# Kernel optimization log

Measured on AMD Instinct MI355X. Metric: run time of the kernel, lower is better.

## Reference

```python
import jax, jax.numpy as jnp
import numpy as np

ALPHA = 0.1
BETA = float(np.log(0.5 / 4 + 1.0))  # theta=0.5, layer=4


def setup_inputs() -> dict:
    key = jax.random.key(0)
    k = jax.random.split(key, 6)
    B, C, N, K = 1, 128, 40000, 16
    x = jax.random.normal(k[0], (B, C, N, 1), dtype=jnp.float32)
    x_0 = jax.random.normal(k[1], (B, N, C), dtype=jnp.float32)
    edge_index = jax.random.randint(k[2], (2, B, N, K), 0, N)
    W1 = jax.random.normal(k[3], (C, C), dtype=jnp.float32) * 0.05
    W2 = jax.random.normal(k[4], (C, C), dtype=jnp.float32) * 0.05
    bias = jax.random.uniform(k[5], (1, 1, C), dtype=jnp.float32)
    return {"x": x, "x_0": x_0, "edge_index": edge_index, "W1": W1, "W2": W2, "bias": bias}


def reference(x, x_0, edge_index, W1, W2, bias):
    # x: [B, C, N, 1]; x_0: [B, N, C]; edge_index: [2, B, N, K]
    B, C, N, _ = x.shape
    idx = edge_index[0]  # neighbor indices [B, N, K]
    self_idx = jnp.broadcast_to(jnp.arange(N, dtype=idx.dtype)[None, :, None], (B, N, 1))
    idx = jnp.concatenate([idx, self_idx], axis=-1)  # add self loops -> [B, N, K+1]
    deg = idx.shape[-1]  # constant degree K+1
    x2 = x[..., 0]  # [B, C, N]
    # irregular gather of neighbor features: [B, C, N, K+1]
    x_j = jax.vmap(lambda xb, ib: xb[:, ib])(x2, idx)
    aggr = x_j.sum(axis=-1) * (1.0 / deg)  # [B, C, N]
    aggr = jnp.swapaxes(aggr, 1, 2)  # [B, N, C]
    out = (aggr * ((1.0 - ALPHA) * (1.0 - BETA))
           + jnp.einsum('bnc,oc->bno', aggr, W1) * BETA
           + x_0 * (ALPHA * (1.0 - BETA))
           + jnp.einsum('bnc,oc->bno', x_0, W2) * BETA
           + bias)
    out = jax.nn.relu(out)
    return jnp.swapaxes(out, 1, 2)[..., None]  # [B, C, N, 1]
```

## Files before the change

### kernel.cpp

```cpp
#include <hip/hip_runtime.h>

#define N_NODES 40000
#define C_DIM   128
#define K_NBR   16

static constexpr float BETA_F = 0.11778303565638346f;
static constexpr float C1_F   = 0.7939952679092549f;
static constexpr float C2_F   = 0.08822169643436166f;

typedef __attribute__((ext_vector_type(8))) short bf16x8;
typedef __attribute__((ext_vector_type(4))) float f32x4;

__device__ __forceinline__ unsigned pack_bf16x2(float a, float b) {
    unsigned ua = __float_as_uint(a), ub = __float_as_uint(b);
    ua += 0x7fffu + ((ua >> 16) & 1u);
    ub += 0x7fffu + ((ub >> 16) & 1u);
    return (ua >> 16) | (ub & 0xffff0000u);
}
__device__ __forceinline__ float bflo(unsigned u) { return __uint_as_float(u << 16); }
__device__ __forceinline__ float bfhi(unsigned u) { return __uint_as_float(u & 0xffff0000u); }

__global__ void build_wfrag_kernel(const float* __restrict__ W1,
                                   const float* __restrict__ W2,
                                   unsigned short* __restrict__ WB) {
    int i = blockIdx.x * 256 + threadIdx.x;
    int frag   = i >> 9;
    int within = i & 511;
    int lane = within >> 3, j = within & 7;
    int otile = frag >> 3, kblk = frag & 7;
    int o = otile * 16 + (lane & 15);
    int c = kblk * 32 + ((lane >> 4) << 3) + j;
    float w = (c < 128) ? W1[o * 128 + c] : W2[o * 128 + c - 128];
    unsigned u = __float_as_uint(w);
    u += 0x7fffu + ((u >> 16) & 1u);
    WB[i] = (unsigned short)(u >> 16);
}

__global__ __launch_bounds__(256) void transpose_cast_kernel(
        const float* __restrict__ x, unsigned* __restrict__ xTb) {
    __shared__ float tile[32][33];
    const int nb = blockIdx.x * 32;
    const int cb = blockIdx.y * 32;
    const int tid = threadIdx.x;
    const int tx = tid & 31, ty = tid >> 5;
#pragma unroll
    for (int i = 0; i < 32; i += 8)
        tile[ty + i][tx] = x[(size_t)(cb + ty + i) * N_NODES + nb + tx];
    __syncthreads();
    const int nl = tid >> 3;
    const int cp = tid & 7;
#pragma unroll
    for (int it = 0; it < 2; ++it) {
        int cpl = cp + 8 * it;
        float a = tile[2 * cpl][nl];
        float b = tile[2 * cpl + 1][nl];
        xTb[(size_t)(nb + nl) * 64 + (cb >> 1) + cpl] = pack_bf16x2(a, b);
    }
}

__global__ __launch_bounds__(256) void fused2_kernel(
        const unsigned* __restrict__ xTb,
        const float*    __restrict__ x0,
        const int*      __restrict__ e0,
        const bf16x8*   __restrict__ WB,
        const float*    __restrict__ bias,
        float*          __restrict__ out) {
    __shared__ unsigned y[32][132];
    __shared__ int eis[512];

    const int nb   = blockIdx.x * 32;
    const int tid  = threadIdx.x;
    const int lane = tid & 63;
    const int wid  = tid >> 6;

    eis[tid]       = e0[(size_t)nb * K_NBR + tid];
    eis[256 + tid] = e0[(size_t)nb * K_NBR + 256 + tid];
    __syncthreads();

    const float inv_deg = 1.0f / 17.0f;
#pragma unroll 1
    for (int s = 0; s < 8; ++s) {
        const int local = wid * 8 + s;
        const int n = nb + local;
        unsigned u = xTb[(size_t)n * 64 + lane];
        float a0 = bflo(u), a1 = bfhi(u);
        const int* ep = &eis[local * K_NBR];
#pragma unroll
        for (int k = 0; k < K_NBR; ++k) {
            const int j = ep[k];
            unsigned v = xTb[(size_t)j * 64 + lane];
            a0 += bflo(v);
            a1 += bfhi(v);
        }
        y[local][lane] = pack_bf16x2(a0 * inv_deg, a1 * inv_deg);
        const float2 xv = *(const float2*)&x0[(size_t)n * C_DIM + 2 * lane];
        y[local][64 + lane] = pack_bf16x2(xv.x, xv.y);
    }
    __syncthreads();

    const int nh = wid & 1;
    const int oh = wid >> 1;
    const int arow = nh * 16 + (lane & 15);
    const int acol = (lane >> 4) * 4;

    bf16x8 afrag[8];
#pragma unroll
    for (int kb = 0; kb < 8; ++kb)
        afrag[kb] = *(const bf16x8*)&y[arow][kb * 16 + acol];

    f32x4 acc[4];
#pragma unroll
    for (int t = 0; t < 4; ++t) {
        f32x4 a = {0.f, 0.f, 0.f, 0.f};
#pragma unroll
        for (int kb = 0; kb < 8; ++kb) {
            bf16x8 b = WB[((oh * 4 + t) * 8 + kb) * 64 + lane];
            a = __builtin_amdgcn_mfma_f32_16x16x32_bf16(afrag[kb], b, a, 0, 0, 0);
        }
        acc[t] = a;
    }

    const int rbase = nh * 16 + (lane >> 4) * 4;
#pragma unroll
    for (int t = 0; t < 4; ++t) {
        const int o = oh * 64 + t * 16 + (lane & 15);
        const float bo = bias[o];
        const int oc = o >> 1;
        const bool hi = (o & 1) != 0;
        float res[4];
#pragma unroll
        for (int r = 0; r < 4; ++r) {
            const int row = rbase + r;
            const unsigned ua = y[row][oc];
            const unsigned ux = y[row][64 + oc];
            const float aggr = hi ? bfhi(ua) : bflo(ua);
            const float x0v  = hi ? bfhi(ux) : bflo(ux);
            float v = fmaf(acc[t][r], BETA_F,
                      fmaf(aggr, C1_F,
                      fmaf(x0v,  C2_F, bo)));
            res[r] = v > 0.0f ? v : 0.0f;
        }
        *(float4*)&out[(size_t)o * N_NODES + nb + rbase] =
            make_float4(res[0], res[1], res[2], res[3]);
    }
}

extern "C" void kernel_launch(void* const* d_in, const int* in_sizes, int n_in,
                              void* d_out, int out_size, void* d_ws, size_t ws_size,
                              hipStream_t stream) {
    const float* x    = (const float*)d_in[0];
    const float* x0   = (const float*)d_in[1];
    const int*   ei   = (const int*)  d_in[2];
    const float* W1   = (const float*)d_in[3];
    const float* W2   = (const float*)d_in[4];
    const float* bias = (const float*)d_in[5];
    float* out = (float*)d_out;

    unsigned short* WB  = (unsigned short*)d_ws;
    unsigned*       xTb = (unsigned*)((char*)d_ws + 65536);

    hipLaunchKernelGGL(build_wfrag_kernel, dim3(128), dim3(256), 0, stream,
                       W1, W2, WB);
    hipLaunchKernelGGL(transpose_cast_kernel, dim3(1250, 4), dim3(256), 0, stream,
                       x, xTb);
    hipLaunchKernelGGL(fused2_kernel, dim3(1250), dim3(256), 0, stream,
                       xTb, x0, ei, (const bf16x8*)WB, bias, out);
}
```

Before: 45.92 us.

## Fold scaling constants into weights, merge prep kernels, widen gather loads

Folds BETA, the 1/17 degree normalization and the C1/C2 identity terms into the bf16 weight matrix, so the epilogue reduces to bias plus ReLU and no longer rereads aggr/x0 from shared memory. Merges the weight-fragment build and the transpose-cast into one prep kernel, removing a launch, and uses float4 loads and uint4 stores for the transpose. In the fused kernel, each half-wave now gathers a separate node with 8-byte loads. Folding the identity terms into bf16 weights lowers the precision of the residual paths, and the single weight-building block may lengthen the prep kernel's tail.

Measured after the change: 67.94 us. +48.0%, slower.

```diff
diff --git a/kernel.cpp b/kernel.cpp
--- a/kernel.cpp
+++ b/kernel.cpp
@@ -4,9 +4,10 @@
 #define C_DIM   128
 #define K_NBR   16
 
-static constexpr float BETA_F = 0.11778303565638346f;
-static constexpr float C1_F   = 0.7939952679092549f;
-static constexpr float C2_F   = 0.08822169643436166f;
+static constexpr float BETA_F  = 0.11778303565638346f;
+static constexpr float C1_F    = 0.7939952679092549f;
+static constexpr float C2_F    = 0.08822169643436166f;
+static constexpr float INV_DEG = 1.0f / 17.0f;
 
 typedef __attribute__((ext_vector_type(8))) short bf16x8;
 typedef __attribute__((ext_vector_type(4))) float f32x4;
@@ -20,45 +21,68 @@
 __device__ __forceinline__ float bflo(unsigned u) { return __uint_as_float(u << 16); }
 __device__ __forceinline__ float bfhi(unsigned u) { return __uint_as_float(u & 0xffff0000u); }
 
-__global__ void build_wfrag_kernel(const float* __restrict__ W1,
-                                   const float* __restrict__ W2,
-                                   unsigned short* __restrict__ WB) {
-    int i = blockIdx.x * 256 + threadIdx.x;
-    int frag   = i >> 9;
-    int within = i & 511;
-    int lane = within >> 3, j = within & 7;
-    int otile = frag >> 3, kblk = frag & 7;
-    int o = otile * 16 + (lane & 15);
-    int c = kblk * 32 + ((lane >> 4) << 3) + j;
-    float w = (c < 128) ? W1[o * 128 + c] : W2[o * 128 + c - 128];
-    unsigned u = __float_as_uint(w);
-    u += 0x7fffu + ((u >> 16) & 1u);
-    WB[i] = (unsigned short)(u >> 16);
+__global__ __launch_bounds__(256) void prep_kernel(
+        const float* __restrict__ x,
+        const float* __restrict__ W1,
+        const float* __restrict__ W2,
+        unsigned* __restrict__ xTb,
+        unsigned short* __restrict__ WB) {
+    __shared__ unsigned tile[64][68];
+
+    if (blockIdx.x == 625) {
+        const int tid = threadIdx.x;
+#pragma unroll 4
+        for (int it = 0; it < 128; ++it) {
+            int i = it * 256 + tid;
+            int frag = i >> 9, within = i & 511;
+            int lane = within >> 3, j = within & 7;
+            int otile = frag >> 3, kblk = frag & 7;
+            int o = otile * 16 + (lane & 15);
+            int c = kblk * 32 + ((lane >> 4) << 3) + j;
+            float v;
+            if (c < 128) {
+                v = (BETA_F * W1[o * 128 + c] + (c == o ? C1_F : 0.0f)) * INV_DEG;
+            } else {
+                int c2 = c - 128;
+                v = BETA_F * W2[o * 128 + c2] + (c2 == o ? C2_F : 0.0f);
+            }
+            unsigned u = __float_as_uint(v);
+            u += 0x7fffu + ((u >> 16) & 1u);
+            WB[i] = (unsigned short)(u >> 16);
+        }
+        return;
+    }
+
+    const int nb = blockIdx.x * 64;
+    const int t  = threadIdx.x;
+    const int p  = t & 63;
+    const int nq = t >> 6;
+
+    const float* r0 = x + (size_t)(2 * p) * N_NODES + nb + nq * 16;
+    const float* r1 = r0 + N_NODES;
+    float4 a[4], b[4];
+#pragma unroll
+    for (int i = 0; i < 4; ++i) {
+        a[i] = *(const float4*)(r0 + 4 * i);
+        b[i] = *(const float4*)(r1 + 4 * i);
+    }
+#pragma unroll
+    for (int i = 0; i < 4; ++i) {
+        tile[nq * 16 + 4 * i + 0][p] = pack_bf16x2(a[i].x, b[i].x);
+        tile[nq * 16 + 4 * i + 1][p] = pack_bf16x2(a[i].y, b[i].y);
+        tile[nq * 16 + 4 * i + 2][p] = pack_bf16x2(a[i].z, b[i].z);
+        tile[nq * 16 + 4 * i + 3][p] = pack_bf16x2(a[i].w, b[i].w);
+    }
+    __syncthreads();
+
+    const int nl = t >> 2, q = t & 3;
+    unsigned* dst = xTb + (size_t)(nb + nl) * 64 + q * 16;
+#pragma unroll
+    for (int jj = 0; jj < 4; ++jj)
+        *(uint4*)(dst + 4 * jj) = *(const uint4*)&tile[nl][q * 16 + 4 * jj];
 }
 
-__global__ __launch_bounds__(256) void transpose_cast_kernel(
-        const float* __restrict__ x, unsigned* __restrict__ xTb) {
-    __shared__ float tile[32][33];
-    const int nb = blockIdx.x * 32;
-    const int cb = blockIdx.y * 32;
-    const int tid = threadIdx.x;
-    const int tx = tid & 31, ty = tid >> 5;
-#pragma unroll
-    for (int i = 0; i < 32; i += 8)
-        tile[ty + i][tx] = x[(size_t)(cb + ty + i) * N_NODES + nb + tx];
-    __syncthreads();
-    const int nl = tid >> 3;
-    const int cp = tid & 7;
-#pragma unroll
-    for (int it = 0; it < 2; ++it) {
-        int cpl = cp + 8 * it;
-        float a = tile[2 * cpl][nl];
-        float b = tile[2 * cpl + 1][nl];
-        xTb[(size_t)(nb + nl) * 64 + (cb >> 1) + cpl] = pack_bf16x2(a, b);
-    }
-}
-
-__global__ __launch_bounds__(256) void fused2_kernel(
+__global__ __launch_bounds__(256) void fused3_kernel(
         const unsigned* __restrict__ xTb,
         const float*    __restrict__ x0,
         const int*      __restrict__ e0,
@@ -77,24 +101,28 @@
     eis[256 + tid] = e0[(size_t)nb * K_NBR + 256 + tid];
     __syncthreads();
 
-    const float inv_deg = 1.0f / 17.0f;
-#pragma unroll 1
-    for (int s = 0; s < 8; ++s) {
-        const int local = wid * 8 + s;
+    const int h  = lane >> 5;
+    const int l5 = lane & 31;
+#pragma unroll 2
+    for (int p4 = 0; p4 < 4; ++p4) {
+        const int local = wid * 8 + p4 * 2 + h;
         const int n = nb + local;
-        unsigned u = xTb[(size_t)n * 64 + lane];
-        float a0 = bflo(u), a1 = bfhi(u);
+        const uint2 sv = *(const uint2*)&xTb[(size_t)n * 64 + 2 * l5];
+        float a0 = bflo(sv.x), a1 = bfhi(sv.x);
+        float a2 = bflo(sv.y), a3 = bfhi(sv.y);
         const int* ep = &eis[local * K_NBR];
 #pragma unroll
         for (int k = 0; k < K_NBR; ++k) {
             const int j = ep[k];
-            unsigned v = xTb[(size_t)j * 64 + lane];
-            a0 += bflo(v);
-            a1 += bfhi(v);
+            const uint2 v = *(const uint2*)&xTb[(size_t)j * 64 + 2 * l5];
+            a0 += bflo(v.x); a1 += bfhi(v.x);
+            a2 += bflo(v.y); a3 += bfhi(v.y);
         }
-        y[local][lane] = pack_bf16x2(a0 * inv_deg, a1 * inv_deg);
-        const float2 xv = *(const float2*)&x0[(size_t)n * C_DIM + 2 * lane];
-        y[local][64 + lane] = pack_bf16x2(xv.x, xv.y);
+        *(uint2*)&y[local][2 * l5] =
+            make_uint2(pack_bf16x2(a0, a1), pack_bf16x2(a2, a3));
+        const float4 xv = *(const float4*)&x0[(size_t)n * C_DIM + 4 * l5];
+        *(uint2*)&y[local][64 + 2 * l5] =
+            make_uint2(pack_bf16x2(xv.x, xv.y), pack_bf16x2(xv.z, xv.w));
     }
     __syncthreads();
 
@@ -125,23 +153,12 @@
     for (int t = 0; t < 4; ++t) {
         const int o = oh * 64 + t * 16 + (lane & 15);
         const float bo = bias[o];
-        const int oc = o >> 1;
-        const bool hi = (o & 1) != 0;
-        float res[4];
-#pragma unroll
-        for (int r = 0; r < 4; ++r) {
-            const int row = rbase + r;
-            const unsigned ua = y[row][oc];
-            const unsigned ux = y[row][64 + oc];
-            const float aggr = hi ? bfhi(ua) : bflo(ua);
-            const float x0v  = hi ? bfhi(ux) : bflo(ux);
-            float v = fmaf(acc[t][r], BETA_F,
-                      fmaf(aggr, C1_F,
-                      fmaf(x0v,  C2_F, bo)));
-            res[r] = v > 0.0f ? v : 0.0f;
-        }
-        *(float4*)&out[(size_t)o * N_NODES + nb + rbase] =
-            make_float4(res[0], res[1], res[2], res[3]);
+        float4 res;
+        res.x = fmaxf(acc[t][0] + bo, 0.0f);
+        res.y = fmaxf(acc[t][1] + bo, 0.0f);
+        res.z = fmaxf(acc[t][2] + bo, 0.0f);
+        res.w = fmaxf(acc[t][3] + bo, 0.0f);
+        *(float4*)&out[(size_t)o * N_NODES + nb + rbase] = res;
     }
 }
 
@@ -159,10 +176,8 @@
     unsigned short* WB  = (unsigned short*)d_ws;
     unsigned*       xTb = (unsigned*)((char*)d_ws + 65536);
 
-    hipLaunchKernelGGL(build_wfrag_kernel, dim3(128), dim3(256), 0, stream,
-                       W1, W2, WB);
-    hipLaunchKernelGGL(transpose_cast_kernel, dim3(1250, 4), dim3(256), 0, stream,
-                       x, xTb);
-    hipLaunchKernelGGL(fused2_kernel, dim3(1250), dim3(256), 0, stream,
+    hipLaunchKernelGGL(prep_kernel, dim3(626), dim3(256), 0, stream,
+                       x, W1, W2, xTb, WB);
+    hipLaunchKernelGGL(fused3_kernel, dim3(1250), dim3(256), 0, stream,
                        xTb, x0, ei, (const bf16x8*)WB, bias, out);
 }
```
